# Kernel tuning notes

Hardware: AMD Instinct MI355X
Metric: run time of the kernel (lower is better)

Reference implementation:

```python
import jax, jax.numpy as jnp
import numpy as np

SCORE_THRESH = 0.05
NMS_THRESH = 0.5
K = 1000            # max NMS candidates (fixed for jit; padded/masked)
IMG_W, IMG_H = 1333, 800


def setup_inputs() -> dict:
    key = jax.random.key(0)
    k1, k2, k3 = jax.random.split(key, 3)
    N, C = 200000, 81
    class_logits = jax.random.normal(k1, (N, C), dtype=jnp.float32) * 2.0
    # well-formed xyxy boxes inside the image
    cxcy = jax.random.uniform(k2, (N, 2), dtype=jnp.float32) * jnp.array([IMG_W, IMG_H], jnp.float32)
    wh = jax.random.uniform(k3, (N, 2), dtype=jnp.float32) * 200.0 + 1.0
    boxes = jnp.concatenate([cxcy - wh * 0.5, cxcy + wh * 0.5], axis=-1)
    return {"class_logits": class_logits, "boxes": boxes}


def _pairwise_iou(b):
    # b: [K, 4] xyxy -> [K, K]
    area = (b[:, 2] - b[:, 0]) * (b[:, 3] - b[:, 1])
    lt = jnp.maximum(b[:, None, :2], b[None, :, :2])
    rb = jnp.minimum(b[:, None, 2:], b[None, :, 2:])
    wh = jnp.clip(rb - lt, 0.0)
    inter = wh[..., 0] * wh[..., 1]
    return inter / (area[:, None] + area[None, :] - inter + 1e-9)


def reference(class_logits, boxes):
    N, C = class_logits.shape
    prob = jax.nn.softmax(class_logits, axis=-1)            # [N, C]
    # clip_to_image (TO_REMOVE=1 convention: clamp to size-1)
    bx = jnp.stack([
        jnp.clip(boxes[:, 0], 0.0, IMG_W - 1),
        jnp.clip(boxes[:, 1], 0.0, IMG_H - 1),
        jnp.clip(boxes[:, 2], 0.0, IMG_W - 1),
        jnp.clip(boxes[:, 3], 0.0, IMG_H - 1),
    ], axis=-1)                                             # [N, 4]
    flat = prob.reshape(-1)                                 # [N*C], class = idx % C
    idx = jnp.arange(N * C)
    valid = (flat > SCORE_THRESH) & (idx % C != 0)          # fg + score threshold
    masked = jnp.where(valid, flat, -jnp.inf)
    top_scores, top_idx = jax.lax.top_k(masked, K)          # sorted descending
    prop_idx = top_idx // C
    cls = top_idx % C
    bk = bx[prop_idx]                                       # [K, 4]
    valid_k = jnp.isfinite(top_scores)
    scores_k = jnp.where(valid_k, top_scores, 0.0)
    # class-aware greedy NMS over the (sorted) top-K candidates
    conflict = (_pairwise_iou(bk) > NMS_THRESH) & (cls[:, None] == cls[None, :])
    rng = jnp.arange(K)

    def body(i, keep):
        sup = jnp.any(keep & conflict[:, i] & (rng < i))
        return keep.at[i].set(keep[i] & ~sup)

    keep = jax.lax.fori_loop(0, K, body, valid_k)
    out = jnp.concatenate([bk, scores_k[:, None]], axis=-1) * keep[:, None].astype(bk.dtype)
    return out  # [K, 5]: (x1, y1, x2, y2, score), zeroed where suppressed/invalid
```

## Files before the change

kernel.cpp:

```cpp
#include <hip/hip_runtime.h>
#include <stdint.h>
#include <math.h>

#define N_CLS    81
#define TOPK     1000
#define LISTCAP  (1u << 21)
#define CAP2     16384
#define SCORE_TH 0.05f
#define IMG_W    1333.0f
#define IMG_H    800.0f
#define GH_REP   8

#define GH_BASE  1905

#define OFF_CNT    0
#define OFF_CNT2   128
#define OFF_TICKA  384
#define OFF_TICKR  640
#define OFF_TICKC  768
#define OFF_GH     1280
#define OFF_RH     5376
#define MEMSET_BYTES 9472
#define OFF_SEL    16768
#define OFF_SEL2   16793984
#define OFF_BOX    16925056
#define OFF_SCORE  16941056
#define OFF_CLS    16945056
#define OFF_MASK   16949056

#define ROWS_PER_BLK 128
#define TILE_FLOATS  (ROWS_PER_BLK * N_CLS)
#define CBUF_CAP     1024
#define TAIL_BLOCKS  128
#define PADK         1016

typedef unsigned long long u64;

__device__ __forceinline__ int ipad(int j) { return j + (j >> 6); }

__device__ __forceinline__ void gload_lds16(const float* g, float* l) {
    __builtin_amdgcn_global_load_lds(
        (const __attribute__((address_space(1))) unsigned int*)g,
        (__attribute__((address_space(3))) unsigned int*)l, 16, 0, 0);
}

__device__ __forceinline__ unsigned agent_load_u32(const unsigned* p) {
    return __hip_atomic_load(p, __ATOMIC_RELAXED, __HIP_MEMORY_SCOPE_AGENT);
}
__device__ __forceinline__ u64 agent_load_u64(const u64* p) {
    return __hip_atomic_load(p, __ATOMIC_RELAXED, __HIP_MEMORY_SCOPE_AGENT);
}
__device__ __forceinline__ void agent_store_u32(unsigned* p, unsigned v) {
    __hip_atomic_store(p, v, __ATOMIC_RELAXED, __HIP_MEMORY_SCOPE_AGENT);
}
__device__ __forceinline__ void agent_store_u64(u64* p, u64 v) {
    __hip_atomic_store(p, v, __ATOMIC_RELAXED, __HIP_MEMORY_SCOPE_AGENT);
}
__device__ __forceinline__ void drain_vm() {
    asm volatile("s_waitcnt vmcnt(0)" ::: "memory");
}

__global__ __launch_bounds__(256) void k_pass1(
        const float* __restrict__ logits, int nrows,
        u64* __restrict__ sel, unsigned* __restrict__ cnt,
        unsigned* __restrict__ ghist) {
    __shared__ float tile[TILE_FLOATS];
    __shared__ unsigned lh[128];
    __shared__ u64 cbuf[CBUF_CAP];
    __shared__ unsigned lcnt, gbase;
    int tid = threadIdx.x, wv = tid >> 6, ln = tid & 63;
    for (int i = tid; i < 128; i += 256) lh[i] = 0;
    if (tid == 0) lcnt = 0;

    int base = blockIdx.x * ROWS_PER_BLK;
    int nr = nrows - base; if (nr > ROWS_PER_BLK) nr = ROWS_PER_BLK;
    const float* gtile = logits + (size_t)base * N_CLS;

    if (nr == ROWS_PER_BLK) {
        #pragma unroll
        for (int it = 0; it < 10; ++it) {
            int c = it * 1024 + wv * 256;
            gload_lds16(gtile + c + ln * 4, tile + c);
        }
        if (tid < TILE_FLOATS - 10240) tile[10240 + tid] = gtile[10240 + tid];
    } else {
        for (int i = tid; i < nr * N_CLS; i += 256) tile[i] = gtile[i];
    }
    __syncthreads();

    int r = tid >> 1, h = tid & 1;
    if (r < nr) {
        const int rb = r * N_CLS + h;
        float v[41];
        #pragma unroll
        for (int m = 0; m < 40; ++m) v[m] = tile[rb + 2 * m];
        v[40] = (h == 0) ? tile[rb + 80] : 0.0f;

        float mx = v[0];
        #pragma unroll
        for (int m = 1; m < 40; ++m) mx = fmaxf(mx, v[m]);
        mx = fmaxf(mx, (h == 0) ? v[40] : v[0]);
        float om = __shfl_xor(mx, 1);
        float mrow = fmaxf(mx, om);

        #pragma unroll
        for (int m = 0; m < 40; ++m) v[m] = expf(v[m] - mrow);
        v[40] = (h == 0) ? expf(v[40] - mrow) : 0.0f;

        float stk0 = 0.f, stk1 = 0.f, stk2 = 0.f, stk3 = 0.f, stk4 = 0.f;
        float S = 0.f;
        #pragma unroll
        for (int i = 0; i < 32; ++i) {
            const int b = ((i & 1) << 4) | ((i & 2) << 2) | (i & 4) |
                          ((i & 8) >> 2) | ((i & 16) >> 4);
            float x = v[b];
            if (b < 8) x += v[b + 32];
            else if (b == 8) x = (h == 0) ? x + v[40] : x;
            if (i & 1) { x = stk0 + x;
              if (i & 2) { x = stk1 + x;
                if (i & 4) { x = stk2 + x;
                  if (i & 8) { x = stk3 + x;
                    if (i & 16) { S = stk4 + x; } else stk4 = x;
                  } else stk3 = x;
                } else stk2 = x;
              } else stk1 = x;
            } else stk0 = x;
        }
        float oS = __shfl_xor(S, 1);
        float s = (h == 0) ? (S + oS) : (oS + S);

        float eth = 0.0499f * s;
        unsigned rowflat = (unsigned)(base + r) * N_CLS + (unsigned)h;
        #pragma unroll
        for (int m = 0; m < 41; ++m) {
            float e = v[m];
            if ((m + h) != 0 && e > eth) {
                float p = e / s;
                if (p > SCORE_TH) {
                    unsigned fb = __float_as_uint(p);
                    atomicAdd(&lh[(fb >> 19) - GH_BASE], 1u);
                    u64 key = ((u64)fb << 32) | (u64)(0xFFFFFFu - (rowflat + 2u * (unsigned)m));
                    unsigned pos = atomicAdd(&lcnt, 1u);
                    if (pos < CBUF_CAP) cbuf[pos] = key;
                    else { unsigned gp = atomicAdd(cnt, 1u); if (gp < LISTCAP) sel[gp] = key; }
                }
            }
        }
    }
    __syncthreads();
    unsigned* gh = ghist + (blockIdx.x & (GH_REP - 1)) * 128;
    for (int i = tid; i < 128; i += 256) {
        unsigned vv = lh[i];
        if (vv) atomicAdd(&gh[i], vv);
    }
    unsigned total = lcnt; if (total > CBUF_CAP) total = CBUF_CAP;
    if (tid == 0) gbase = atomicAdd(cnt, total);
    __syncthreads();
    unsigned gb = gbase;
    for (unsigned i = tid; i < total; i += 256) {
        unsigned gp = gb + i;
        if (gp < LISTCAP) sel[gp] = cbuf[i];
    }
}

__global__ __launch_bounds__(1024) void k_tail(
        char* __restrict__ ws, const float* __restrict__ boxes,
        float* __restrict__ out) {
    unsigned* cnt   = (unsigned*)(ws + OFF_CNT);
    unsigned* cnt2  = (unsigned*)(ws + OFF_CNT2);
    unsigned* tickA = (unsigned*)(ws + OFF_TICKA);
    unsigned* tickR = (unsigned*)(ws + OFF_TICKR);
    unsigned* tickC = (unsigned*)(ws + OFF_TICKC);
    unsigned* ghist = (unsigned*)(ws + OFF_GH);
    unsigned* rhist = (unsigned*)(ws + OFF_RH);
    u64*      sel   = (u64*)(ws + OFF_SEL);
    u64*      sel2  = (u64*)(ws + OFF_SEL2);
    u64*      boxB  = (u64*)(ws + OFF_BOX);
    unsigned* scrB  = (unsigned*)(ws + OFF_SCORE);
    unsigned* clsB  = (unsigned*)(ws + OFF_CLS);
    u64*      mask  = (u64*)(ws + OFF_MASK);

    __shared__ unsigned scu[1024], sfu[1024];
    __shared__ union {
        unsigned lhist[1024];
        struct {
            float x1[PADK], y1[PADK], x2[PADK], y2[PADK];
            int cls[PADK]; unsigned sc[PADK];
        } c;
    } shu;
    __shared__ u64 words[16];
    __shared__ int schanged, swB;
    __shared__ unsigned swCA, stk, stb;

    int tid = threadIdx.x, ln = tid & 63;
    unsigned nb = gridDim.x;

    if (tid < 128) {
        unsigned c = 0;
        #pragma unroll
        for (int rr = 0; rr < GH_REP; ++rr) c += ghist[rr * 128 + tid];
        scu[tid] = c; sfu[tid] = c;
    }
    if (tid == 0) swB = -1;
    __syncthreads();
    #pragma unroll
    for (int off = 1; off < 128; off <<= 1) {
        unsigned a = 0;
        if (tid < 128) a = (tid + off < 128) ? sfu[tid + off] : 0u;
        __syncthreads();
        if (tid < 128) sfu[tid] += a;
        __syncthreads();
    }
    if (tid == 0) swCA = sfu[0];
    __syncthreads();
    if (tid < 128) {
        unsigned incl = sfu[tid], excl = incl - scu[tid];
        if (excl < TOPK && incl >= TOPK) { swB = tid; swCA = excl; }
    }
    __syncthreads();
    int B = swB;
    unsigned CA = swCA;
    unsigned M = *cnt; if (M > LISTCAP) M = LISTCAP;
    unsigned stride = nb * 1024u;
    unsigned tbc = (B < 0) ? 0u : ((unsigned)(B + GH_BASE) << 19);
    unsigned Bbits = (unsigned)(B + GH_BASE);

    shu.lhist[tid] = 0;
    __syncthreads();
    for (unsigned ibase = blockIdx.x * 1024u; ibase < M; ibase += stride) {
        unsigned i = ibase + tid;
        bool act = (i < M);
        u64 key = act ? sel[i] : 0ull;
        unsigned bv = (unsigned)(key >> 32);
        if (act && B >= 0 && (bv >> 19) == Bbits)
            atomicAdd(&shu.lhist[(bv >> 9) & 1023u], 1u);
        bool c = act && (bv >= tbc) && (key != 0ull);
        u64 b = __ballot(c);
        int n = __popcll(b);
        if (n) {
            unsigned wb = 0;
            if (ln == 0) wb = atomicAdd(cnt2, (unsigned)n);
            wb = __shfl(wb, 0);
            if (c) {
                unsigned pos = wb + (unsigned)__popcll(b & ((1ull << ln) - 1ull));
                if (pos < CAP2) agent_store_u64(&sel2[pos], key);
            }
        }
    }
    __syncthreads();
    { unsigned vv = shu.lhist[tid]; if (vv) atomicAdd(&rhist[tid], vv); }
    __syncthreads();
    drain_vm();
    if (tid == 0) {
        atomicAdd(tickA, 1u);
        unsigned v;
        do { __builtin_amdgcn_s_sleep(2); v = agent_load_u32(tickA); } while (v < nb);
    }
    __syncthreads();

    unsigned tb = 0;
    {
        unsigned c = (B >= 0) ? agent_load_u32(&rhist[tid]) : 0u;
        scu[tid] = c; sfu[tid] = c;
        if (tid == 0) stb = 0;
        __syncthreads();
        #pragma unroll
        for (int off = 1; off < 1024; off <<= 1) {
            unsigned a = (tid + off < 1024) ? sfu[tid + off] : 0u;
            __syncthreads();
            sfu[tid] += a;
            __syncthreads();
        }
        unsigned incl = sfu[tid], excl = incl - scu[tid];
        if (B >= 0 && CA + excl < TOPK && CA + incl >= TOPK)
            stb = ((unsigned)(B + GH_BASE) << 19) | ((unsigned)tid << 9);
        __syncthreads();
        tb = stb;
    }

    {
        unsigned S = agent_load_u32(cnt2); if (S > CAP2) S = CAP2;
        unsigned slot = blockIdx.x * 16u + (unsigned)(tid >> 6);
        unsigned nslots = nb * 16u;
        unsigned lim = (S > TOPK) ? S : TOPK;
        for (unsigned k = slot; k < lim; k += nslots) {
            if (k < S) {
                u64 my = agent_load_u64(&sel2[k]);
                if ((unsigned)(my >> 32) < tb) continue;
                unsigned rk = 0;
                for (unsigned j = ln; j < S; j += 64)
                    rk += (agent_load_u64(&sel2[j]) > my) ? 1u : 0u;
                #pragma unroll
                for (int off = 32; off > 0; off >>= 1) rk += __shfl_xor(rk, off);
                if (ln == 0 && rk < TOPK) {
                    float sc = __uint_as_float((unsigned)(my >> 32));
                    unsigned fi = 0xFFFFFFu - (unsigned)(my & 0xFFFFFFFFull);
                    unsigned prop = fi / N_CLS;
                    int cls = (int)(fi - prop * N_CLS);
                    const float* bx = boxes + (size_t)prop * 4;
                    float x1 = fminf(fmaxf(bx[0], 0.0f), IMG_W - 1.0f);
                    float y1 = fminf(fmaxf(bx[1], 0.0f), IMG_H - 1.0f);
                    float x2 = fminf(fmaxf(bx[2], 0.0f), IMG_W - 1.0f);
                    float y2 = fminf(fmaxf(bx[3], 0.0f), IMG_H - 1.0f);
                    agent_store_u64(&boxB[rk * 2],
                        ((u64)__float_as_uint(y1) << 32) | __float_as_uint(x1));
                    agent_store_u64(&boxB[rk * 2 + 1],
                        ((u64)__float_as_uint(y2) << 32) | __float_as_uint(x2));
                    agent_store_u32(&scrB[rk], __float_as_uint(sc));
                    agent_store_u32(&clsB[rk], (unsigned)cls);
                }
            } else if (ln == 0) {
                agent_store_u64(&boxB[k * 2], 0ull);
                agent_store_u64(&boxB[k * 2 + 1], 0ull);
                agent_store_u32(&scrB[k], 0u);
                agent_store_u32(&clsB[k], (unsigned)-1);
            }
        }
    }
    __syncthreads();
    drain_vm();
    if (tid == 0) stk = atomicAdd(tickR, 1u);
    __syncthreads();
    if (blockIdx.x >= 16) return;
    if (tid == 0) {
        unsigned v;
        do { __builtin_amdgcn_s_sleep(2); v = agent_load_u32(tickR); } while (v < nb);
    }
    __syncthreads();

    if (tid < TOPK) {
        u64 a = agent_load_u64(&boxB[tid * 2]);
        u64 b = agent_load_u64(&boxB[tid * 2 + 1]);
        int ip = ipad(tid);
        shu.c.x1[ip] = __uint_as_float((unsigned)a);
        shu.c.y1[ip] = __uint_as_float((unsigned)(a >> 32));
        shu.c.x2[ip] = __uint_as_float((unsigned)b);
        shu.c.y2[ip] = __uint_as_float((unsigned)(b >> 32));
        shu.c.cls[ip] = (int)agent_load_u32(&clsB[tid]);
        shu.c.sc[ip]  = agent_load_u32(&scrB[tid]);
    }
    __syncthreads();
    {
        int t = blockIdx.x * 1024 + tid;
        int i = t >> 4, w = t & 15;
        if (i < TOPK) {
            int ip = ipad(i);
            float x1 = shu.c.x1[ip], y1 = shu.c.y1[ip];
            float x2 = shu.c.x2[ip], y2 = shu.c.y2[ip];
            int ci = shu.c.cls[ip];
            float ai = (x2 - x1) * (y2 - y1);
            u64 m = 0;
            int jbase = w << 6;
            for (int jj = 0; jj < 64; jj++) {
                int j = jbase + jj;
                if (j >= TOPK) break;
                int jp = ipad(j);
                float u1 = shu.c.x1[jp], w1 = shu.c.y1[jp];
                float u2 = shu.c.x2[jp], w2 = shu.c.y2[jp];
                float aj = (u2 - u1) * (w2 - w1);
                float ww = fmaxf(fminf(x2, u2) - fmaxf(x1, u1), 0.0f);
                float hh = fmaxf(fminf(y2, w2) - fmaxf(y1, w1), 0.0f);
                float inter = ww * hh;
                float iou = inter / (ai + aj - inter + 1e-9f);
                if (iou > 0.5f && ci == shu.c.cls[jp]) m |= (1ull << jj);
            }
            agent_store_u64(&mask[(size_t)i * 16 + w], m);
        }
    }
    __syncthreads();
    drain_vm();
    if (tid == 0) stk = atomicAdd(tickC, 1u);
    __syncthreads();
    if (stk != 15u) return;

    int wvv = tid >> 6;
    int myip = ipad(tid < TOPK ? tid : 0);
    bool valid = (tid < TOPK) && (__uint_as_float(shu.c.sc[myip]) > 0.0f);
    u64 row[16];
    #pragma unroll
    for (int w = 0; w < 16; w++)
        row[w] = (tid < TOPK) ? agent_load_u64(&mask[(size_t)tid * 16 + w]) : 0ull;
    u64 lowmask = (1ull << ln) - 1ull;
    bool keep = valid;
    for (int it = 0; it < 1024; ++it) {
        u64 b = __ballot(keep);
        if (ln == 0) words[wvv] = b;
        if (tid == 0) schanged = 0;
        __syncthreads();
        u64 sup = 0;
        for (int w = 0; w <= wvv; w++) {
            u64 kw = words[w];
            if (w == wvv) kw &= lowmask;
            sup |= row[w] & kw;
        }
        bool nk = valid && (sup == 0ull);
        if (nk != keep) schanged = 1;
        keep = nk;
        __syncthreads();
        if (!schanged) break;
    }
    if (tid < TOPK) {
        float sc = __uint_as_float(shu.c.sc[myip]);
        out[tid * 5 + 0] = keep ? shu.c.x1[myip] : 0.0f;
        out[tid * 5 + 1] = keep ? shu.c.y1[myip] : 0.0f;
        out[tid * 5 + 2] = keep ? shu.c.x2[myip] : 0.0f;
        out[tid * 5 + 3] = keep ? shu.c.y2[myip] : 0.0f;
        out[tid * 5 + 4] = keep ? sc : 0.0f;
    }
}

extern "C" void kernel_launch(void* const* d_in, const int* in_sizes, int n_in,
                              void* d_out, int out_size, void* d_ws, size_t ws_size,
                              hipStream_t stream) {
    const float* logits = (const float*)d_in[0];
    const float* boxes  = (const float*)d_in[1];
    float* out = (float*)d_out;
    int nrows = in_sizes[0] / N_CLS;

    char* w = (char*)d_ws;
    unsigned* cnt   = (unsigned*)(w + OFF_CNT);
    unsigned* ghist = (unsigned*)(w + OFF_GH);
    u64* sel        = (u64*)(w + OFF_SEL);

    hipMemsetAsync(w, 0, MEMSET_BYTES, stream);

    int nblk = (nrows + ROWS_PER_BLK - 1) / ROWS_PER_BLK;
    k_pass1<<<nblk, 256, 0, stream>>>(logits, nrows, sel, cnt, ghist);
    k_tail<<<TAIL_BLOCKS, 1024, 0, stream>>>(w, boxes, out);
}
```

Before: 184.7 us.

## Compute NMS mask in one block and resolve suppression wave-by-wave

Instead of spreading the IoU mask across 16 blocks, writing it to global memory and using a second ticket barrier, block 0 alone computes each candidate's 16 mask words directly into registers. The global fixed-point NMS iteration, which needed block-wide syncs on every pass, becomes a sequential sweep over the 16 waves. Each wave finds its own keep set through ballot-only fixed-point iteration once earlier waves are final. This removes a global round trip and a cross-block barrier, but puts the whole 1000x1000 IoU computation on a single block and serialises the waves.

```diff
diff --git a/kernel.cpp b/kernel.cpp
--- a/kernel.cpp
+++ b/kernel.cpp
@@ -17,7 +17,6 @@
 #define OFF_CNT2   128
 #define OFF_TICKA  384
 #define OFF_TICKR  640
-#define OFF_TICKC  768
 #define OFF_GH     1280
 #define OFF_RH     5376
 #define MEMSET_BYTES 9472
@@ -26,7 +25,6 @@
 #define OFF_BOX    16925056
 #define OFF_SCORE  16941056
 #define OFF_CLS    16945056
-#define OFF_MASK   16949056
 
 #define ROWS_PER_BLK 128
 #define TILE_FLOATS  (ROWS_PER_BLK * N_CLS)
@@ -170,7 +168,6 @@
     unsigned* cnt2  = (unsigned*)(ws + OFF_CNT2);
     unsigned* tickA = (unsigned*)(ws + OFF_TICKA);
     unsigned* tickR = (unsigned*)(ws + OFF_TICKR);
-    unsigned* tickC = (unsigned*)(ws + OFF_TICKC);
     unsigned* ghist = (unsigned*)(ws + OFF_GH);
     unsigned* rhist = (unsigned*)(ws + OFF_RH);
     u64*      sel   = (u64*)(ws + OFF_SEL);
@@ -178,7 +175,6 @@
     u64*      boxB  = (u64*)(ws + OFF_BOX);
     unsigned* scrB  = (unsigned*)(ws + OFF_SCORE);
     unsigned* clsB  = (unsigned*)(ws + OFF_CLS);
-    u64*      mask  = (u64*)(ws + OFF_MASK);
 
     __shared__ unsigned scu[1024], sfu[1024];
     __shared__ union {
@@ -189,7 +185,7 @@
         } c;
     } shu;
     __shared__ u64 words[16];
-    __shared__ int schanged, swB;
+    __shared__ int swB;
     __shared__ unsigned swCA, stk, stb;
 
     int tid = threadIdx.x, ln = tid & 63;
@@ -321,7 +317,7 @@
     drain_vm();
     if (tid == 0) stk = atomicAdd(tickR, 1u);
     __syncthreads();
-    if (blockIdx.x >= 16) return;
+    if (blockIdx.x != 0) return;
     if (tid == 0) {
         unsigned v;
         do { __builtin_amdgcn_s_sleep(2); v = agent_load_u32(tickR); } while (v < nb);
@@ -340,15 +336,16 @@
         shu.c.sc[ip]  = agent_load_u32(&scrB[tid]);
     }
     __syncthreads();
+
+    u64 row[16];
     {
-        int t = blockIdx.x * 1024 + tid;
-        int i = t >> 4, w = t & 15;
-        if (i < TOPK) {
-            int ip = ipad(i);
-            float x1 = shu.c.x1[ip], y1 = shu.c.y1[ip];
-            float x2 = shu.c.x2[ip], y2 = shu.c.y2[ip];
-            int ci = shu.c.cls[ip];
-            float ai = (x2 - x1) * (y2 - y1);
+        int ip = ipad(tid < TOPK ? tid : 0);
+        float x1 = shu.c.x1[ip], y1 = shu.c.y1[ip];
+        float x2 = shu.c.x2[ip], y2 = shu.c.y2[ip];
+        int ci = shu.c.cls[ip];
+        float ai = (x2 - x1) * (y2 - y1);
+        #pragma unroll
+        for (int w = 0; w < 16; ++w) {
             u64 m = 0;
             int jbase = w << 6;
             for (int jj = 0; jj < 64; jj++) {
@@ -364,41 +361,33 @@
                 float iou = inter / (ai + aj - inter + 1e-9f);
                 if (iou > 0.5f && ci == shu.c.cls[jp]) m |= (1ull << jj);
             }
-            agent_store_u64(&mask[(size_t)i * 16 + w], m);
-        }
-    }
-    __syncthreads();
-    drain_vm();
-    if (tid == 0) stk = atomicAdd(tickC, 1u);
-    __syncthreads();
-    if (stk != 15u) return;
+            row[w] = (tid < TOPK) ? m : 0ull;
+        }
+    }
 
     int wvv = tid >> 6;
     int myip = ipad(tid < TOPK ? tid : 0);
     bool valid = (tid < TOPK) && (__uint_as_float(shu.c.sc[myip]) > 0.0f);
-    u64 row[16];
-    #pragma unroll
-    for (int w = 0; w < 16; w++)
-        row[w] = (tid < TOPK) ? agent_load_u64(&mask[(size_t)tid * 16 + w]) : 0ull;
     u64 lowmask = (1ull << ln) - 1ull;
-    bool keep = valid;
-    for (int it = 0; it < 1024; ++it) {
-        u64 b = __ballot(keep);
-        if (ln == 0) words[wvv] = b;
-        if (tid == 0) schanged = 0;
+    bool keep = false;
+    for (int w = 0; w < 16; ++w) {
+        if (wvv == w) {
+            u64 ext = 0;
+            for (int u = 0; u < w; ++u) ext |= row[u] & words[u];
+            bool k = valid && (ext == 0ull);
+            u64 K = __ballot(k), Kp;
+            int guard = 0;
+            do {
+                Kp = K;
+                k = valid && (ext == 0ull) && ((row[w] & Kp & lowmask) == 0ull);
+                K = __ballot(k);
+            } while (K != Kp && ++guard < 64);
+            if (ln == 0) words[w] = K;
+            keep = k;
+        }
         __syncthreads();
-        u64 sup = 0;
-        for (int w = 0; w <= wvv; w++) {
-            u64 kw = words[w];
-            if (w == wvv) kw &= lowmask;
-            sup |= row[w] & kw;
-        }
-        bool nk = valid && (sup == 0ull);
-        if (nk != keep) schanged = 1;
-        keep = nk;
-        __syncthreads();
-        if (!schanged) break;
-    }
+    }
+
     if (tid < TOPK) {
         float sc = __uint_as_float(shu.c.sc[myip]);
         out[tid * 5 + 0] = keep ? shu.c.x1[myip] : 0.0f;
```

Measured after the change: 356.5 us. 93.0% more time.
